# Kernel tuning notes

Hardware: AMD Instinct MI355X
Metric: run time of the kernel (lower is better)

The kernel has to match this reference:

```python
import jax, jax.numpy as jnp
import numpy as np

NEG_SLOPE = 0.2  # PyG GATConv default leaky_relu slope
EPS = 1e-16


def gat_conv(x, W, att_src, att_dst, bias, src, dst, num_nodes, heads, out_ch, concat):
    # x: [N, F_in]; W: [F_in, heads*out_ch]
    h = (x @ W).reshape(num_nodes, heads, out_ch)          # [N, H, C]
    a_src = jnp.sum(h * att_src, axis=-1)                  # [N, H]
    a_dst = jnp.sum(h * att_dst, axis=-1)                  # [N, H]
    alpha = jax.nn.leaky_relu(a_src[src] + a_dst[dst], NEG_SLOPE)  # [E, H]
    # segment softmax over incoming edges of each destination node
    amax = jax.ops.segment_max(alpha, dst, num_segments=num_nodes)  # [N, H]
    ex = jnp.exp(alpha - amax[dst])                        # [E, H]
    denom = jax.ops.segment_sum(ex, dst, num_segments=num_nodes)    # [N, H]
    attn = ex / (denom[dst] + EPS)                         # [E, H]
    msg = h[src] * attn[:, :, None]                        # [E, H, C]
    out = jax.ops.segment_sum(msg, dst, num_segments=num_nodes)     # [N, H, C]
    if concat:
        out = out.reshape(num_nodes, heads * out_ch)
    else:
        out = out.mean(axis=1)
    return out + bias


def setup_inputs() -> dict:
    key = jax.random.key(0)
    ks = jax.random.split(key, 10)
    N, E, F_in, H, C, OUT = 50000, 800000, 512, 4, 64, 40
    x = jax.random.normal(ks[0], (N, F_in), dtype=jnp.float32)
    edge_index = jax.random.randint(ks[1], (2, E), 0, N, dtype=jnp.int64)
    s1 = (2.0 / (F_in + H * C)) ** 0.5
    s2 = (2.0 / (H * C + OUT)) ** 0.5
    return {
        "x": x,
        "edge_index": edge_index,
        "W1": jax.random.normal(ks[2], (F_in, H * C), dtype=jnp.float32) * s1,
        "att_src1": jax.random.normal(ks[3], (H, C), dtype=jnp.float32) * 0.1,
        "att_dst1": jax.random.normal(ks[4], (H, C), dtype=jnp.float32) * 0.1,
        "b1": jnp.zeros((H * C,), dtype=jnp.float32),
        "W2": jax.random.normal(ks[5], (H * C, OUT), dtype=jnp.float32) * s2,
        "att_src2": jax.random.normal(ks[6], (1, OUT), dtype=jnp.float32) * 0.1,
        "att_dst2": jax.random.normal(ks[7], (1, OUT), dtype=jnp.float32) * 0.1,
        "b2": jnp.zeros((OUT,), dtype=jnp.float32),
    }


def reference(x, edge_index, W1, att_src1, att_dst1, b1, W2, att_src2, att_dst2, b2):
    N = x.shape[0]
    H, C = att_src1.shape
    OUT = att_src2.shape[1]
    # PyG GATConv default: add self-loops
    loops = jnp.arange(N, dtype=edge_index.dtype)
    src = jnp.concatenate([edge_index[0], loops])
    dst = jnp.concatenate([edge_index[1], loops])
    # dropout is identity in eval mode
    h = gat_conv(x, W1, att_src1, att_dst1, b1, src, dst, N, H, C, concat=True)
    h = jax.nn.elu(h)
    out = gat_conv(h, W2, att_src2, att_dst2, b2, src, dst, N, 1, OUT, concat=False)
    return jax.nn.log_softmax(out, axis=1)
```

## Files before the change

kernel.cpp:

```cpp
#include <hip/hip_runtime.h>
#include <math.h>

#define FIN   512
#define H1DIM 256
#define HEADS 4
#define CH    64
#define OUTC  40
#define NEG   0.2f
#define EPSV  1e-16f
#define BK    64

__device__ __forceinline__ float leaky(float a) { return fmaxf(a, NEG * a); }

__device__ __forceinline__ short f2bf(float f) {
    unsigned u = __builtin_bit_cast(unsigned, f);
    u += 0x7FFFu + ((u >> 16) & 1u);
    return (short)(u >> 16);
}
__device__ __forceinline__ float bf2f(short s) {
    return __builtin_bit_cast(float, ((unsigned)(unsigned short)s) << 16);
}
__device__ __forceinline__ unsigned cvtpk(float lo, float hi) {
    unsigned r;
    asm("v_cvt_pk_bf16_f32 %0, %1, %2" : "=v"(r) : "v"(lo), "v"(hi));
    return r;
}
__device__ __forceinline__ float lo16(unsigned u) {
    return __builtin_bit_cast(float, u << 16);
}
__device__ __forceinline__ float hi16(unsigned u) {
    return __builtin_bit_cast(float, u & 0xffff0000u);
}

typedef __attribute__((ext_vector_type(2))) float floatx2;

__device__ __forceinline__ unsigned f32x2_to_fp8x2(float a, float b) {
    return (unsigned)__builtin_amdgcn_cvt_pk_fp8_f32(a, b, 0, false);
}
template <bool HI>
__device__ __forceinline__ floatx2 fp8x2_to_f32(unsigned u) {
    return __builtin_amdgcn_cvt_pk_f32_fp8((int)u, HI);
}

typedef __attribute__((ext_vector_type(8))) short short8;
typedef __attribute__((ext_vector_type(4))) short short4_t;
typedef __attribute__((ext_vector_type(4))) float float4_t;

typedef unsigned int u32;
typedef const __attribute__((address_space(1))) u32 gu32;
typedef __attribute__((address_space(3))) u32 lu32;

__device__ __forceinline__ void load_lds16(const void* g, void* l) {
    __builtin_amdgcn_global_load_lds((gu32*)g, (lu32*)l, 16, 0, 0);
}

__global__ void cvt_w1_kernel(const float* __restrict__ W1, short* __restrict__ w1t)
{
    int idx = blockIdx.x * 256 + threadIdx.x;
    if (idx >= FIN * H1DIM) return;
    int k = idx >> 8;
    int n = idx & 255;
    w1t[(size_t)n * FIN + k] = f2bf(W1[idx]);
}

__global__ __launch_bounds__(256, 4) void gemm1_mfma_kernel(
    const float* __restrict__ x, const short* __restrict__ w1t,
    const float* __restrict__ attS, const float* __restrict__ attD,
    unsigned char* __restrict__ h1f, float* __restrict__ aS1, float* __restrict__ aD1, int N)
{
    __shared__ float Alf[2][64 * BK];

    const int tid  = threadIdx.x;
    const int lane = tid & 63;
    const int wid  = tid >> 6;
    const int row0 = blockIdx.x * 64;
    const int col0 = wid * 64;
    const int quad = lane >> 4;
    const int m16  = lane & 15;

    const int achunk = ((tid & 15) ^ (tid >> 4)) * 4;
    const float* asrcA[4];
#pragma unroll
    for (int p = 0; p < 4; ++p) {
        int r = row0 + p * 16 + (tid >> 4);
        if (r >= N) r = N - 1;
        asrcA[p] = x + (size_t)r * FIN + achunk;
    }

    const short* bp[4];
#pragma unroll
    for (int j = 0; j < 4; ++j)
        bp[j] = w1t + (size_t)(col0 + j * 16 + m16) * FIN + quad * 8;

    float4_t acc[4][4];
#pragma unroll
    for (int i = 0; i < 4; ++i)
#pragma unroll
        for (int j = 0; j < 4; ++j) acc[i][j] = (float4_t){0.f, 0.f, 0.f, 0.f};

#pragma unroll
    for (int p = 0; p < 4; ++p)
        load_lds16(asrcA[p], Alf[0] + p * 1024 + tid * 4);

#pragma unroll
    for (int kk = 0; kk < FIN / BK; ++kk) {
        const int k0 = kk * BK;

        short8 b[2][4];
#pragma unroll
        for (int half = 0; half < 2; ++half)
#pragma unroll
            for (int j = 0; j < 4; ++j)
                b[half][j] = *(const short8*)(bp[j] + k0 + half * 32);

        if (kk < FIN / BK - 1) {
#pragma unroll
            for (int p = 0; p < 4; ++p)
                load_lds16(asrcA[p] + k0 + BK, Alf[(kk + 1) & 1] + p * 1024 + tid * 4);
            asm volatile("s_waitcnt vmcnt(12)" ::: "memory");
        } else {
            asm volatile("s_waitcnt vmcnt(8)" ::: "memory");
        }
        __builtin_amdgcn_sched_barrier(0);
        __builtin_amdgcn_s_barrier();
        __builtin_amdgcn_sched_barrier(0);

        const float* Acur = Alf[kk & 1];
#pragma unroll
        for (int half = 0; half < 2; ++half) {
            short8 a[4];
#pragma unroll
            for (int i = 0; i < 4; ++i) {
                int row = i * 16 + m16;
                int c0 = (quad + 4 * half) * 2;
                float4 f0 = *(const float4*)&Acur[row * BK + ((c0 ^ m16) * 4)];
                float4 f1 = *(const float4*)&Acur[row * BK + (((c0 + 1) ^ m16) * 4)];
                unsigned* tp = (unsigned*)&a[i];
                tp[0] = cvtpk(f0.x, f0.y);
                tp[1] = cvtpk(f0.z, f0.w);
                tp[2] = cvtpk(f1.x, f1.y);
                tp[3] = cvtpk(f1.z, f1.w);
            }
#pragma unroll
            for (int i = 0; i < 4; ++i)
#pragma unroll
                for (int j = 0; j < 4; ++j)
                    acc[i][j] = __builtin_amdgcn_mfma_f32_16x16x32_bf16(a[i], b[half][j], acc[i][j], 0, 0, 0);
        }
        __builtin_amdgcn_sched_barrier(0);
        __builtin_amdgcn_s_barrier();
        __builtin_amdgcn_sched_barrier(0);
    }

    float attSv[4], attDv[4];
#pragma unroll
    for (int j = 0; j < 4; ++j) {
        attSv[j] = attS[col0 + j * 16 + m16];
        attDv[j] = attD[col0 + j * 16 + m16];
    }

#pragma unroll
    for (int i = 0; i < 4; ++i) {
#pragma unroll
        for (int r = 0; r < 4; ++r) {
            int row = row0 + i * 16 + quad * 4 + r;
            if (row < N) {
                unsigned pa = f32x2_to_fp8x2(acc[i][0][r], acc[i][1][r]);
                unsigned pb = f32x2_to_fp8x2(acc[i][2][r], acc[i][3][r]);
                unsigned char* hp = h1f + (size_t)row * H1DIM + col0 + m16;
                hp[0]  = (unsigned char)(pa & 0xff);
                hp[16] = (unsigned char)((pa >> 8) & 0xff);
                hp[32] = (unsigned char)(pb & 0xff);
                hp[48] = (unsigned char)((pb >> 8) & 0xff);
            }
            float ps = acc[i][0][r] * attSv[0] + acc[i][1][r] * attSv[1]
                     + acc[i][2][r] * attSv[2] + acc[i][3][r] * attSv[3];
            float pd = acc[i][0][r] * attDv[0] + acc[i][1][r] * attDv[1]
                     + acc[i][2][r] * attDv[2] + acc[i][3][r] * attDv[3];
#pragma unroll
            for (int off = 1; off < 16; off <<= 1) {
                ps += __shfl_xor(ps, off);
                pd += __shfl_xor(pd, off);
            }
            if (m16 == 0 && row < N) {
                aS1[(size_t)row * 4 + wid] = ps;
                aD1[(size_t)row * 4 + wid] = pd;
            }
        }
    }
}

__global__ void degcount_kernel(const int* __restrict__ ei, int* __restrict__ deg,
                                int* __restrict__ rank, int E, int Etot)
{
    int e = blockIdx.x * 256 + threadIdx.x;
    if (e >= Etot) return;
    int d = (e < E) ? ei[E + e] : (e - E);
    rank[e] = atomicAdd(&deg[d], 1);
}

__global__ __launch_bounds__(1024) void scan_partial_kernel(
    const int* __restrict__ deg, int* __restrict__ offsets,
    int* __restrict__ bsums, int N)
{
    __shared__ int wsums[16];
    __shared__ int excl[16];
    int tid = threadIdx.x, lane = tid & 63, wid = tid >> 6;
    int idx = blockIdx.x * 1024 + tid;
    int v = (idx < N) ? deg[idx] : 0;
    int sv = v;
#pragma unroll
    for (int off = 1; off < 64; off <<= 1) {
        int t = __shfl_up(sv, off, 64);
        if (lane >= off) sv += t;
    }
    if (lane == 63) wsums[wid] = sv;
    __syncthreads();
    if (wid == 0 && lane < 16) {
        int wv = wsums[lane];
        int sw = wv;
#pragma unroll
        for (int off = 1; off < 16; off <<= 1) {
            int t = __shfl_up(sw, off, 64);
            if (lane >= off) sw += t;
        }
        excl[lane] = sw - wv;
        if (lane == 15) bsums[blockIdx.x] = sw;
    }
    __syncthreads();
    if (idx < N) offsets[idx + 1] = sv + excl[wid];
}

__global__ __launch_bounds__(1024) void scan_tops_kernel(
    int* __restrict__ bsums, int* __restrict__ boffs, int nb)
{
    __shared__ int wsums[16];
    __shared__ int excl[16];
    int tid = threadIdx.x, lane = tid & 63, wid = tid >> 6;
    int v = (tid < nb) ? bsums[tid] : 0;
    int sv = v;
#pragma unroll
    for (int off = 1; off < 64; off <<= 1) {
        int t = __shfl_up(sv, off, 64);
        if (lane >= off) sv += t;
    }
    if (lane == 63) wsums[wid] = sv;
    __syncthreads();
    if (wid == 0 && lane < 16) {
        int wv = wsums[lane];
        int sw = wv;
#pragma unroll
        for (int off = 1; off < 16; off <<= 1) {
            int t = __shfl_up(sw, off, 64);
            if (lane >= off) sw += t;
        }
        excl[lane] = sw - wv;
    }
    __syncthreads();
    if (tid < nb) boffs[tid] = sv + excl[wid] - v;
}

__global__ __launch_bounds__(1024) void scan_add_kernel(
    int* __restrict__ offsets, const int* __restrict__ boffs, int N)
{
    int idx = blockIdx.x * 1024 + threadIdx.x;
    if (idx == 0) offsets[0] = 0;
    if (idx < N) offsets[idx + 1] += boffs[blockIdx.x];
}

__global__ void scatter_kernel(const int* __restrict__ ei, const int* __restrict__ offsets,
                               const int* __restrict__ rank, int* __restrict__ csr_src,
                               int E, int Etot)
{
    int e = blockIdx.x * 256 + threadIdx.x;
    if (e >= Etot) return;
    int s, d;
    if (e < E) { s = ei[e]; d = ei[E + e]; }
    else       { s = e - E; d = s; }
    csr_src[offsets[d] + rank[e]] = s;
}

__global__ __launch_bounds__(256) void agg1_kernel(
    const unsigned char* __restrict__ h1f, const float* __restrict__ aS,
    const float* __restrict__ aD, const int* __restrict__ offsets,
    const int* __restrict__ csr_src, const float* __restrict__ b1,
    short* __restrict__ g1b, int N)
{
    int lane = threadIdx.x & 63, wid = threadIdx.x >> 6;
    int half = lane >> 5;
    int l32  = lane & 31;
    int n = blockIdx.x * 4 + wid;
    if (n >= N) return;
    int start = offsets[n], end = offsets[n + 1];
    int h = l32 >> 3;
    int cbase = l32 * 8;
    float adh = aD[(size_t)n * 4 + h];

    float ac[8];
#pragma unroll
    for (int c = 0; c < 8; ++c) ac[c] = 0.f;
    float denom = 0.f;

    int p = start;
    for (; p + 4 <= end; p += 4) {
        int sA0 = csr_src[p],     sB0 = csr_src[p + 1];
        int sA1 = csr_src[p + 2], sB1 = csr_src[p + 3];
        int s0 = half ? sB0 : sA0;
        int s1 = half ? sB1 : sA1;
        float t0 = aS[(size_t)s0 * 4 + h] + adh;
        float t1 = aS[(size_t)s1 * 4 + h] + adh;
        uint2 r0 = *(const uint2*)&h1f[(size_t)s0 * H1DIM + cbase];
        uint2 r1 = *(const uint2*)&h1f[(size_t)s1 * H1DIM + cbase];
        float w0 = __expf(leaky(t0));
        float w1 = __expf(leaky(t1));
        denom += w0 + w1;
        floatx2 d0a = fp8x2_to_f32<false>(r0.x), d0b = fp8x2_to_f32<true>(r0.x);
        floatx2 d0c = fp8x2_to_f32<false>(r0.y), d0d = fp8x2_to_f32<true>(r0.y);
        floatx2 d1a = fp8x2_to_f32<false>(r1.x), d1b = fp8x2_to_f32<true>(r1.x);
        floatx2 d1c = fp8x2_to_f32<false>(r1.y), d1d = fp8x2_to_f32<true>(r1.y);
        ac[0] += w0 * d0a.x + w1 * d1a.x;
        ac[1] += w0 * d0a.y + w1 * d1a.y;
        ac[2] += w0 * d0b.x + w1 * d1b.x;
        ac[3] += w0 * d0b.y + w1 * d1b.y;
        ac[4] += w0 * d0c.x + w1 * d1c.x;
        ac[5] += w0 * d0c.y + w1 * d1c.y;
        ac[6] += w0 * d0d.x + w1 * d1d.x;
        ac[7] += w0 * d0d.y + w1 * d1d.y;
    }
    for (; p + 2 <= end; p += 2) {
        int sA = csr_src[p], sB = csr_src[p + 1];
        int s = half ? sB : sA;
        float t = aS[(size_t)s * 4 + h] + adh;
        uint2 r = *(const uint2*)&h1f[(size_t)s * H1DIM + cbase];
        float w = __expf(leaky(t));
        denom += w;
        floatx2 da = fp8x2_to_f32<false>(r.x), db = fp8x2_to_f32<true>(r.x);
        floatx2 dc = fp8x2_to_f32<false>(r.y), dd = fp8x2_to_f32<true>(r.y);
        ac[0] += w * da.x; ac[1] += w * da.y;
        ac[2] += w * db.x; ac[3] += w * db.y;
        ac[4] += w * dc.x; ac[5] += w * dc.y;
        ac[6] += w * dd.x; ac[7] += w * dd.y;
    }
    if (p < end) {
        int s = csr_src[p];
        float t = aS[(size_t)s * 4 + h] + adh;
        uint2 r = *(const uint2*)&h1f[(size_t)s * H1DIM + cbase];
        float w = half ? 0.f : __expf(leaky(t));
        denom += w;
        floatx2 da = fp8x2_to_f32<false>(r.x), db = fp8x2_to_f32<true>(r.x);
        floatx2 dc = fp8x2_to_f32<false>(r.y), dd = fp8x2_to_f32<true>(r.y);
        ac[0] += w * da.x; ac[1] += w * da.y;
        ac[2] += w * db.x; ac[3] += w * db.y;
        ac[4] += w * dc.x; ac[5] += w * dc.y;
        ac[6] += w * dd.x; ac[7] += w * dd.y;
    }

    denom += __shfl_xor(denom, 32);
#pragma unroll
    for (int c = 0; c < 8; ++c) ac[c] += __shfl_xor(ac[c], 32);

    if (half == 0) {
        float inv = 1.f / (denom + EPSV);
        float4 b0 = *(const float4*)&b1[cbase];
        float4 b4 = *(const float4*)&b1[cbase + 4];
        float v[8];
        v[0] = ac[0] * inv + b0.x;
        v[1] = ac[1] * inv + b0.y;
        v[2] = ac[2] * inv + b0.z;
        v[3] = ac[3] * inv + b0.w;
        v[4] = ac[4] * inv + b4.x;
        v[5] = ac[5] * inv + b4.y;
        v[6] = ac[6] * inv + b4.z;
        v[7] = ac[7] * inv + b4.w;
#pragma unroll
        for (int c = 0; c < 8; ++c) v[c] = v[c] > 0.f ? v[c] : expm1f(v[c]);
        short8 o;
        unsigned* op = (unsigned*)&o;
        op[0] = cvtpk(v[0], v[1]);
        op[1] = cvtpk(v[2], v[3]);
        op[2] = cvtpk(v[4], v[5]);
        op[3] = cvtpk(v[6], v[7]);
        *(short8*)&g1b[(size_t)n * H1DIM + cbase] = o;
    }
}

__global__ __launch_bounds__(256) void gemm2_kernel(
    const short* __restrict__ g1b, const float* __restrict__ W2,
    const float* __restrict__ attS2, const float* __restrict__ attD2,
    short* __restrict__ h2b, float* __restrict__ aS2, float* __restrict__ aD2, int N)
{
    __shared__ float rows[4][8][256];
    int lane = threadIdx.x & 63, wid = threadIdx.x >> 6;
    int nbase = blockIdx.x * 32 + wid * 8;
    bool act = lane < OUTC;
    int cc = act ? lane : 0;
    float attS = act ? attS2[lane] : 0.f;
    float attD = act ? attD2[lane] : 0.f;

#pragma unroll
    for (int i = 0; i < 8; ++i) {
        int n = nbase + i;
        float4 v = make_float4(0.f, 0.f, 0.f, 0.f);
        if (n < N) {
            short4_t hv = *(const short4_t*)&g1b[(size_t)n * H1DIM + lane * 4];
            v = make_float4(bf2f(hv[0]), bf2f(hv[1]), bf2f(hv[2]), bf2f(hv[3]));
        }
        *(float4*)&rows[wid][i][lane * 4] = v;
    }

    float acc[8];
#pragma unroll
    for (int i = 0; i < 8; ++i) acc[i] = 0.f;

    for (int k = 0; k < H1DIM; k += 4) {
        float w0 = W2[(size_t)(k + 0) * OUTC + cc];
        float w1 = W2[(size_t)(k + 1) * OUTC + cc];
        float w2 = W2[(size_t)(k + 2) * OUTC + cc];
        float w3 = W2[(size_t)(k + 3) * OUTC + cc];
#pragma unroll
        for (int i = 0; i < 8; ++i) {
            float4 g = *(const float4*)&rows[wid][i][k];
            acc[i] += g.x * w0 + g.y * w1 + g.z * w2 + g.w * w3;
        }
    }

#pragma unroll
    for (int i = 0; i < 8; ++i) {
        int n = nbase + i;
        if (n >= N) continue;
        if (act) h2b[(size_t)n * OUTC + lane] = f2bf(acc[i]);
        float ts = act ? acc[i] * attS : 0.f;
        float td = act ? acc[i] * attD : 0.f;
#pragma unroll
        for (int off = 32; off > 0; off >>= 1) {
            ts += __shfl_xor(ts, off);
            td += __shfl_xor(td, off);
        }
        if (lane == 0) { aS2[n] = ts; aD2[n] = td; }
    }
}

__global__ __launch_bounds__(256) void agg2_kernel(
    const short* __restrict__ h2b, const float* __restrict__ aS2,
    const float* __restrict__ aD2, const int* __restrict__ offsets,
    const int* __restrict__ csr_src, const float* __restrict__ b2,
    float* __restrict__ out, int N)
{
    int lane = threadIdx.x & 63, wid = threadIdx.x >> 6;
    int n = blockIdx.x * 4 + wid;
    if (n >= N) return;
    int start = offsets[n], end = offsets[n + 1];
    bool act = lane < OUTC;
    int cc = act ? lane : 0;
    float ad = aD2[n];

    float acc = 0.f, denom = 0.f;
    int p = start;
    for (; p + 4 <= end; p += 4) {
        int s0 = csr_src[p], s1 = csr_src[p + 1], s2 = csr_src[p + 2], s3 = csr_src[p + 3];
        float w0 = __expf(leaky(aS2[s0] + ad));
        float w1 = __expf(leaky(aS2[s1] + ad));
        float w2 = __expf(leaky(aS2[s2] + ad));
        float w3 = __expf(leaky(aS2[s3] + ad));
        short v0 = h2b[(size_t)s0 * OUTC + cc];
        short v1 = h2b[(size_t)s1 * OUTC + cc];
        short v2 = h2b[(size_t)s2 * OUTC + cc];
        short v3 = h2b[(size_t)s3 * OUTC + cc];
        denom += w0 + w1 + w2 + w3;
        acc += w0 * bf2f(v0) + w1 * bf2f(v1) + w2 * bf2f(v2) + w3 * bf2f(v3);
    }
    for (; p < end; ++p) {
        int s = csr_src[p];
        float w = __expf(leaky(aS2[s] + ad));
        denom += w;
        acc += w * bf2f(h2b[(size_t)s * OUTC + cc]);
    }

    float v = acc / (denom + EPSV) + (act ? b2[lane] : 0.f);

    float vm = act ? v : -INFINITY;
#pragma unroll
    for (int off = 32; off > 0; off >>= 1) vm = fmaxf(vm, __shfl_xor(vm, off));
    float ex2 = act ? __expf(v - vm) : 0.f;
    float tot = ex2;
#pragma unroll
    for (int off = 32; off > 0; off >>= 1) tot += __shfl_xor(tot, off);
    float res = v - vm - __logf(tot);
    if (act) out[(size_t)n * OUTC + lane] = res;
}

extern "C" void kernel_launch(void* const* d_in, const int* in_sizes, int n_in,
                              void* d_out, int out_size, void* d_ws, size_t ws_size,
                              hipStream_t stream)
{
    const float* x     = (const float*)d_in[0];
    const int*   ei    = (const int*)d_in[1];
    const float* W1    = (const float*)d_in[2];
    const float* attS1 = (const float*)d_in[3];
    const float* attD1 = (const float*)d_in[4];
    const float* b1    = (const float*)d_in[5];
    const float* W2    = (const float*)d_in[6];
    const float* attS2 = (const float*)d_in[7];
    const float* attD2 = (const float*)d_in[8];
    const float* b2    = (const float*)d_in[9];
    float* out = (float*)d_out;

    const int N    = in_sizes[0] / FIN;
    const int E    = in_sizes[1] / 2;
    const int Etot = E + N;
    const int nb   = (N + 1023) / 1024;

    char* ws = (char*)d_ws;
    size_t off = 0;
    auto take = [&](size_t bytes) -> char* {
        char* p = ws + off;
        off = (off + bytes + 255) & ~(size_t)255;
        return p;
    };
    unsigned char* h1f = (unsigned char*)take((size_t)N * H1DIM);
    short* g1b     = (short*)take((size_t)N * H1DIM * 2);
    short* w1t     = (short*)take((size_t)FIN * H1DIM * 2);
    float* aS1     = (float*)take((size_t)N * 4 * 4);
    float* aD1     = (float*)take((size_t)N * 4 * 4);
    short* h2b     = (short*)take((size_t)N * OUTC * 2);
    float* aS2v    = (float*)take((size_t)N * 4);
    float* aD2v    = (float*)take((size_t)N * 4);
    int*   deg     = (int*)take((size_t)N * 4);
    int*   offsets = (int*)take((size_t)(N + 1) * 4);
    int*   bsums   = (int*)take((size_t)nb * 4);
    int*   boffs   = (int*)take((size_t)nb * 4);
    int*   rank    = (int*)take((size_t)Etot * 4);
    int*   csr_src = (int*)take((size_t)Etot * 4);

    (void)hipMemsetAsync(deg, 0, (size_t)N * 4, stream);

    cvt_w1_kernel<<<(FIN * H1DIM + 255) / 256, 256, 0, stream>>>(W1, w1t);
    gemm1_mfma_kernel<<<(N + 63) / 64, 256, 0, stream>>>(x, w1t, attS1, attD1, h1f, aS1, aD1, N);
    degcount_kernel<<<(Etot + 255) / 256, 256, 0, stream>>>(ei, deg, rank, E, Etot);
    scan_partial_kernel<<<nb, 1024, 0, stream>>>(deg, offsets, bsums, N);
    scan_tops_kernel<<<1, 1024, 0, stream>>>(bsums, boffs, nb);
    scan_add_kernel<<<nb, 1024, 0, stream>>>(offsets, boffs, N);
    scatter_kernel<<<(Etot + 255) / 256, 256, 0, stream>>>(ei, offsets, rank, csr_src, E, Etot);
    agg1_kernel<<<(N + 3) / 4, 256, 0, stream>>>(h1f, aS1, aD1, offsets, csr_src, b1, g1b, N);
    gemm2_kernel<<<(N + 31) / 32, 256, 0, stream>>>(g1b, W2, attS2, attD2, h2b, aS2v, aD2v, N);
    agg2_kernel<<<(N + 3) / 4, 256, 0, stream>>>(h2b, aS2v, aD2v, offsets, csr_src, b2, out, N);
}
```

Measured before the change: 411.1 us.

## Load full A row-tile into LDS, prefetch B in registers, stage fp8 output

Rewrites the first-layer GEMM so each block loads its whole 64x512 fp32 slice of x into a swizzled 128KB LDS buffer in one go. This replaces the double-buffered per-K-step loads and removes the per-iteration barriers. B fragments are software-prefetched one K step ahead in registers. The fp8 output tile is staged through LDS and written with coalesced 16-byte stores instead of scattered byte stores. The large LDS footprint limits the kernel to one block per CU, and compute can no longer overlap the A loads within a block.

After: 427.1 us. +3.9%, slower.

```diff
diff --git a/kernel.cpp b/kernel.cpp
--- a/kernel.cpp
+++ b/kernel.cpp
@@ -63,12 +63,12 @@
     w1t[(size_t)n * FIN + k] = f2bf(W1[idx]);
 }
 
-__global__ __launch_bounds__(256, 4) void gemm1_mfma_kernel(
+__global__ __launch_bounds__(256, 1) void gemm1_mfma_kernel(
     const float* __restrict__ x, const short* __restrict__ w1t,
     const float* __restrict__ attS, const float* __restrict__ attD,
     unsigned char* __restrict__ h1f, float* __restrict__ aS1, float* __restrict__ aD1, int N)
 {
-    __shared__ float Alf[2][64 * BK];
+    __shared__ float As[64 * 512];
 
     const int tid  = threadIdx.x;
     const int lane = tid & 63;
@@ -78,14 +78,15 @@
     const int quad = lane >> 4;
     const int m16  = lane & 15;
 
-    const int achunk = ((tid & 15) ^ (tid >> 4)) * 4;
-    const float* asrcA[4];
-#pragma unroll
-    for (int p = 0; p < 4; ++p) {
-        int r = row0 + p * 16 + (tid >> 4);
-        if (r >= N) r = N - 1;
-        asrcA[p] = x + (size_t)r * FIN + achunk;
-    }
+#pragma unroll
+    for (int inst = 0; inst < 32; ++inst) {
+        int c   = inst * 256 + tid;
+        int row = c >> 7;
+        int q   = (c & 127) ^ (row & 7);
+        int gr  = row0 + row; if (gr >= N) gr = N - 1;
+        load_lds16(x + (size_t)gr * FIN + q * 4, (char*)As + c * 16);
+    }
+    __syncthreads();
 
     const short* bp[4];
 #pragma unroll
@@ -98,43 +99,33 @@
 #pragma unroll
         for (int j = 0; j < 4; ++j) acc[i][j] = (float4_t){0.f, 0.f, 0.f, 0.f};
 
-#pragma unroll
-    for (int p = 0; p < 4; ++p)
-        load_lds16(asrcA[p], Alf[0] + p * 1024 + tid * 4);
+    short8 bcur[2][4];
+#pragma unroll
+    for (int half = 0; half < 2; ++half)
+#pragma unroll
+        for (int j = 0; j < 4; ++j)
+            bcur[half][j] = *(const short8*)(bp[j] + half * 32);
 
 #pragma unroll
     for (int kk = 0; kk < FIN / BK; ++kk) {
-        const int k0 = kk * BK;
-
-        short8 b[2][4];
-#pragma unroll
-        for (int half = 0; half < 2; ++half)
-#pragma unroll
-            for (int j = 0; j < 4; ++j)
-                b[half][j] = *(const short8*)(bp[j] + k0 + half * 32);
-
+        short8 bnext[2][4];
         if (kk < FIN / BK - 1) {
 #pragma unroll
-            for (int p = 0; p < 4; ++p)
-                load_lds16(asrcA[p] + k0 + BK, Alf[(kk + 1) & 1] + p * 1024 + tid * 4);
-            asm volatile("s_waitcnt vmcnt(12)" ::: "memory");
-        } else {
-            asm volatile("s_waitcnt vmcnt(8)" ::: "memory");
-        }
-        __builtin_amdgcn_sched_barrier(0);
-        __builtin_amdgcn_s_barrier();
-        __builtin_amdgcn_sched_barrier(0);
-
-        const float* Acur = Alf[kk & 1];
+            for (int half = 0; half < 2; ++half)
+#pragma unroll
+                for (int j = 0; j < 4; ++j)
+                    bnext[half][j] = *(const short8*)(bp[j] + (kk + 1) * BK + half * 32);
+        }
 #pragma unroll
         for (int half = 0; half < 2; ++half) {
             short8 a[4];
 #pragma unroll
             for (int i = 0; i < 4; ++i) {
                 int row = i * 16 + m16;
-                int c0 = (quad + 4 * half) * 2;
-                float4 f0 = *(const float4*)&Acur[row * BK + ((c0 ^ m16) * 4)];
-                float4 f1 = *(const float4*)&Acur[row * BK + (((c0 + 1) ^ m16) * 4)];
+                int cb  = kk * 16 + (quad + 4 * half) * 2;
+                const char* rp = (const char*)As + row * 2048;
+                float4 f0 = *(const float4*)(rp + ((cb ^ (row & 7)) * 16));
+                float4 f1 = *(const float4*)(rp + (((cb + 1) ^ (row & 7)) * 16));
                 unsigned* tp = (unsigned*)&a[i];
                 tp[0] = cvtpk(f0.x, f0.y);
                 tp[1] = cvtpk(f0.z, f0.w);
@@ -145,11 +136,15 @@
             for (int i = 0; i < 4; ++i)
 #pragma unroll
                 for (int j = 0; j < 4; ++j)
-                    acc[i][j] = __builtin_amdgcn_mfma_f32_16x16x32_bf16(a[i], b[half][j], acc[i][j], 0, 0, 0);
-        }
-        __builtin_amdgcn_sched_barrier(0);
-        __builtin_amdgcn_s_barrier();
-        __builtin_amdgcn_sched_barrier(0);
+                    acc[i][j] = __builtin_amdgcn_mfma_f32_16x16x32_bf16(a[i], bcur[half][j], acc[i][j], 0, 0, 0);
+        }
+        if (kk < FIN / BK - 1) {
+#pragma unroll
+            for (int half = 0; half < 2; ++half)
+#pragma unroll
+                for (int j = 0; j < 4; ++j)
+                    bcur[half][j] = bnext[half][j];
+        }
     }
 
     float attSv[4], attDv[4];
@@ -159,20 +154,22 @@
         attDv[j] = attD[col0 + j * 16 + m16];
     }
 
+    __syncthreads();
+    unsigned char* Asb = (unsigned char*)As;
+
 #pragma unroll
     for (int i = 0; i < 4; ++i) {
 #pragma unroll
         for (int r = 0; r < 4; ++r) {
-            int row = row0 + i * 16 + quad * 4 + r;
-            if (row < N) {
-                unsigned pa = f32x2_to_fp8x2(acc[i][0][r], acc[i][1][r]);
-                unsigned pb = f32x2_to_fp8x2(acc[i][2][r], acc[i][3][r]);
-                unsigned char* hp = h1f + (size_t)row * H1DIM + col0 + m16;
-                hp[0]  = (unsigned char)(pa & 0xff);
-                hp[16] = (unsigned char)((pa >> 8) & 0xff);
-                hp[32] = (unsigned char)(pb & 0xff);
-                hp[48] = (unsigned char)((pb >> 8) & 0xff);
-            }
+            int rloc = i * 16 + quad * 4 + r;
+            unsigned pa = f32x2_to_fp8x2(acc[i][0][r], acc[i][1][r]);
+            unsigned pb = f32x2_to_fp8x2(acc[i][2][r], acc[i][3][r]);
+            int cb = rloc * 256 + col0 + m16;
+            Asb[cb]      = (unsigned char)(pa & 0xff);
+            Asb[cb + 16] = (unsigned char)((pa >> 8) & 0xff);
+            Asb[cb + 32] = (unsigned char)(pb & 0xff);
+            Asb[cb + 48] = (unsigned char)((pb >> 8) & 0xff);
+
             float ps = acc[i][0][r] * attSv[0] + acc[i][1][r] * attSv[1]
                      + acc[i][2][r] * attSv[2] + acc[i][3][r] * attSv[3];
             float pd = acc[i][0][r] * attDv[0] + acc[i][1][r] * attDv[1]
@@ -182,11 +179,21 @@
                 ps += __shfl_xor(ps, off);
                 pd += __shfl_xor(pd, off);
             }
+            int row = row0 + rloc;
             if (m16 == 0 && row < N) {
                 aS1[(size_t)row * 4 + wid] = ps;
                 aD1[(size_t)row * 4 + wid] = pd;
             }
         }
+    }
+    __syncthreads();
+
+#pragma unroll
+    for (int inst = 0; inst < 4; ++inst) {
+        int flat = inst * 4096 + tid * 16;
+        int row  = flat >> 8;
+        if (row0 + row < N)
+            *(float4*)(h1f + (size_t)row0 * H1DIM + flat) = *(const float4*)(Asb + flat);
     }
 }
 
```
